# Performance work log

Measured on AMD Instinct MI355X. Metric: run time of the kernel, lower is better.

The kernel has to match this reference:

```python
import jax, jax.numpy as jnp
import numpy as np

K = 8192        # nodes (radio links)
DEG = 32        # out-degree per node
E = K * DEG
GE = 8          # graph_embedding_size
VAR = np.float32((10.0 ** (-19.9) * 5e6) / 10.0)  # output_noise_power / tx_power


def _init_mlp(key, dims_list):
    # per-node stacked Linear params, torch default init U(-1/sqrt(fan_in), 1/sqrt(fan_in))
    params = []
    for (din, dout) in dims_list:
        key, k1, k2 = jax.random.split(key, 3)
        b = float(1.0 / np.sqrt(din))
        params.append(jax.random.uniform(k1, (K, din, dout), minval=-b, maxval=b, dtype=jnp.float32))
        params.append(jax.random.uniform(k2, (K, dout), minval=-b, maxval=b, dtype=jnp.float32))
    return params


def setup_inputs() -> dict:
    key = jax.random.key(0)
    k = jax.random.split(key, 8)
    # edges sorted by src, exactly DEG distinct non-self out-neighbors per node
    src = jnp.repeat(jnp.arange(K), DEG)
    gaps = jax.random.randint(k[0], (K, DEG), 1, (K - 1) // DEG + 1)
    dst = ((jnp.arange(K)[:, None] + jnp.cumsum(gaps, axis=1)) % K).reshape(-1)
    edge_index = jnp.stack([src, dst])
    x = jax.random.uniform(k[1], (K, 1 + GE), dtype=jnp.float32)
    edge_attr = jax.random.uniform(k[2], (E, 1), dtype=jnp.float32)
    H = jax.random.uniform(k[3], (K, K), dtype=jnp.float32) * 1e-12  # |h_ij|^2 gains
    Wm1, bm1, Wm2, bm2 = _init_mlp(k[4], [(2 + GE, 32), (32, 32)])
    Wu1, bu1, Wu2, bu2 = _init_mlp(k[5], [(33 + GE, 16), (16, GE)])
    Wh1, bh1, Wh2, bh2 = _init_mlp(k[6], [(GE, 16), (16, 1)])
    return dict(x=x, edge_attr=edge_attr, H=H, edge_index=edge_index,
                Wm1=Wm1, bm1=bm1, Wm2=Wm2, bm2=bm2,
                Wu1=Wu1, bu1=bu1, Wu2=Wu2, bu2=bu2,
                Wh1=Wh1, bh1=bh1, Wh2=Wh2, bh2=bh2)


def reference(x, edge_attr, H, edge_index,
              Wm1, bm1, Wm2, bm2, Wu1, bu1, Wu2, bu2, Wh1, bh1, Wh2, bh2):
    src, dst = edge_index[0], edge_index[1]

    def conv(x):
        # message: tmp_e = [x[src_e], edge_attr_e]; node src's private mlp_m.
        # edges are contiguous groups of DEG per src -> grouped GEMM as batched einsum
        tmp = jnp.concatenate([x[src], edge_attr], axis=1).reshape(K, DEG, 2 + GE)
        h = jax.nn.relu(jnp.einsum('ked,kdh->keh', tmp, Wm1) + bm1[:, None])
        msg = jax.nn.relu(jnp.einsum('ked,kdh->keh', h, Wm2) + bm2[:, None])
        aggr = msg.sum(axis=1)                                  # [K,32] sum-aggregate
        t = jnp.concatenate([x, aggr], axis=1)                  # [K,41]
        u = jax.nn.relu(jnp.einsum('kd,kdh->kh', t, Wu1) + bu1)
        comb = jax.nn.relu(jnp.einsum('kd,kdh->kh', u, Wu2) + bu2)  # [K,8]
        return jnp.concatenate([x[:, :1], comb], axis=1)        # keep direct-channel col

    x3 = conv(conv(conv(x)))                                    # 3 rounds of LocalConv
    emb = x3[:, 1:]                                             # [K,8]
    hh = jax.nn.relu(jnp.einsum('kd,kdh->kh', emb, Wh1) + bh1)
    p = jax.nn.sigmoid(jnp.einsum('kd,kdh->kh', hh, Wh2) + bh2)[:, 0]  # power in (0,1)

    # per-node (negative) local rate over 1-hop out-neighborhood
    valid = p * jnp.diagonal(H)                                 # p_i * |h_ii|^2
    interf = jax.ops.segment_sum(p[dst] * H[src, dst], src, num_segments=K) + VAR
    interf = jax.lax.stop_gradient(interf)                      # .detach() in original
    local_rate = -jnp.log2(1.0 + valid / interf)                # [K]
    return local_rate
```

## Files before the change

kernel.cpp:

```cpp
#include <hip/hip_runtime.h>
#include <hip/hip_bf16.h>
#include <math.h>

#define KN 8192
#define DEG 32
#define EE (KN*DEG)

#define VAR_F 6.294627058970831e-15f

typedef __attribute__((ext_vector_type(8)))  short bf16x8;
typedef __attribute__((ext_vector_type(16))) float f32x16;

static __device__ __forceinline__ short bf_hi(float f) {
    __hip_bfloat16 h = __float2bfloat16(f);
    return __builtin_bit_cast(short, h);
}
static __device__ __forceinline__ float bf_f(short s) {
    __hip_bfloat16 h = __builtin_bit_cast(__hip_bfloat16, s);
    return __bfloat162float(h);
}

__global__ __launch_bounds__(64, 4) void mpnn_fused(
    const float* __restrict__ x,
    const float* __restrict__ edge_attr,
    const float* __restrict__ H,
    const int* __restrict__ edge_index,
    const float* __restrict__ Wm1, const float* __restrict__ bm1,
    const float* __restrict__ Wm2, const float* __restrict__ bm2,
    const float* __restrict__ Wu1, const float* __restrict__ bu1,
    const float* __restrict__ Wu2, const float* __restrict__ bu2,
    const float* __restrict__ Wh1, const float* __restrict__ bh1,
    const float* __restrict__ Wh2, const float* __restrict__ bh2,
    float* __restrict__ p_ws, float* __restrict__ valid_ws,
    float* __restrict__ hv_ws)
{
    __shared__ __align__(16) float c_lds[32];
    __shared__ float xt[44];
    __shared__ float ubuf[16];

    const int lane = threadIdx.x;
    const int col  = lane & 31;
    const int g    = lane >> 5;
    const int k    = blockIdx.x;

    const int m  = lane & 15;
    const int dg = lane >> 4;
    const int o  = lane & 7;
    const int mg = lane >> 3;

    const int* dstp = edge_index + EE;
    const int dv = dstp[k*DEG + col];
    const float Hv    = H[(size_t)k*KN + dv];
    const float Hdiag = H[(size_t)k*KN + k];

    const float a_e = edge_attr[k*32 + col];

    float wm1v[5];
    #pragma unroll
    for (int t = 0; t < 5; ++t) wm1v[t] = Wm1[(size_t)k*320 + t*64 + lane];

    float w9v[16];
    {
        const float* w9p = Wm1 + (size_t)k*320 + 288;
        float4 wa = *(const float4*)(w9p + g*8);
        float4 wb = *(const float4*)(w9p + g*8 + 4);
        float4 wc = *(const float4*)(w9p + 16 + g*8);
        float4 wd = *(const float4*)(w9p + 16 + g*8 + 4);
        w9v[0]=wa.x;  w9v[1]=wa.y;  w9v[2]=wa.z;  w9v[3]=wa.w;
        w9v[4]=wb.x;  w9v[5]=wb.y;  w9v[6]=wb.z;  w9v[7]=wb.w;
        w9v[8]=wc.x;  w9v[9]=wc.y;  w9v[10]=wc.z; w9v[11]=wc.w;
        w9v[12]=wd.x; w9v[13]=wd.y; w9v[14]=wd.z; w9v[15]=wd.w;
    }

    float wm2f[16];
    #pragma unroll
    for (int s = 0; s < 2; ++s)
        #pragma unroll
        for (int i = 0; i < 8; ++i)
            wm2f[s*8+i] = Wm2[(size_t)k*1024 + (s*16 + g*8 + i)*32 + col];

    const float bm1_i = bm1[k*32 + col];
    const float bm2_i = bm2[k*32 + col];

    float wu1v[10];
    #pragma unroll
    for (int t = 0; t < 10; ++t) wu1v[t] = Wu1[(size_t)k*656 + t*64 + lane];
    float wu1t = 0.f;
    if (lane < 16) wu1t = Wu1[(size_t)k*656 + 640 + lane];
    const float bu1_m = bu1[k*16 + m];

    const float wu2a  = Wu2[(size_t)k*128 + (mg*2+0)*8 + o];
    const float wu2b  = Wu2[(size_t)k*128 + (mg*2+1)*8 + o];
    const float bu2_o = bu2[k*8 + o];

    float wh1v[2];
    #pragma unroll
    for (int t = 0; t < 2; ++t) wh1v[t] = Wh1[(size_t)k*128 + t*64 + lane];
    const float bh1_m = bh1[k*16 + m];
    const float wh2_m = Wh2[k*16 + m];
    const float bh2_k = bh2[k];

    if (lane < 9) xt[lane] = x[(size_t)k*9 + lane];

    if (g == 0) hv_ws[k*DEG + col] = Hv;
    if (lane == 0) valid_ws[KN + k] = Hdiag;

    bf16x8 Bhi[2], Blo[2];
    #pragma unroll
    for (int s = 0; s < 2; ++s) {
        #pragma unroll
        for (int i = 0; i < 8; ++i) {
            float wv = wm2f[s*8+i];
            short h = bf_hi(wv);
            Bhi[s][i] = h;
            Blo[s][i] = bf_hi(wv - bf_f(h));
        }
    }

    for (int it = 0; it < 3; ++it) {
        float cpart = 0.f;
        #pragma unroll
        for (int t = 0; t < 4; ++t) cpart = fmaf(xt[2*t + g], wm1v[t], cpart);
        if (g == 0) cpart = fmaf(xt[8], wm1v[4], cpart);
        float c = bm1_i + cpart + __shfl_xor(cpart, 32);
        if (g == 0) c_lds[col] = c;

        const float4* cb = (const float4*)c_lds;
        float4 q0 = cb[g*2 + 0];
        float4 q1 = cb[g*2 + 1];
        float4 q2 = cb[4 + g*2 + 0];
        float4 q3 = cb[4 + g*2 + 1];
        float cv[16] = {q0.x,q0.y,q0.z,q0.w, q1.x,q1.y,q1.z,q1.w,
                        q2.x,q2.y,q2.z,q2.w, q3.x,q3.y,q3.z,q3.w};
        bf16x8 Ahi[2], Alo[2];
        #pragma unroll
        for (int s = 0; s < 2; ++s) {
            #pragma unroll
            for (int i = 0; i < 8; ++i) {
                int t = s*8 + i;
                float hv = fmaxf(fmaf(a_e, w9v[t], cv[t]), 0.f);
                short h = bf_hi(hv);
                Ahi[s][i] = h;
                Alo[s][i] = bf_hi(hv - bf_f(h));
            }
        }

        f32x16 acc;
        #pragma unroll
        for (int rr = 0; rr < 16; ++rr) acc[rr] = 0.f;
        #pragma unroll
        for (int s = 0; s < 2; ++s) {
            acc = __builtin_amdgcn_mfma_f32_32x32x16_bf16(Ahi[s], Bhi[s], acc, 0, 0, 0);
            acc = __builtin_amdgcn_mfma_f32_32x32x16_bf16(Ahi[s], Blo[s], acc, 0, 0, 0);
            acc = __builtin_amdgcn_mfma_f32_32x32x16_bf16(Alo[s], Bhi[s], acc, 0, 0, 0);
        }

        float ag = 0.f;
        #pragma unroll
        for (int rr = 0; rr < 16; ++rr) ag += fmaxf(acc[rr] + bm2_i, 0.f);
        ag += __shfl_xor(ag, 32);
        if (g == 0) xt[9 + col] = ag;

        float up = 0.f;
        #pragma unroll
        for (int t = 0; t < 10; ++t) up = fmaf(xt[4*t + dg], wu1v[t], up);
        up = fmaf(xt[40], wu1t, up);
        up += __shfl_xor(up, 16);
        up += __shfl_xor(up, 32);
        float u = fmaxf(up + bu1_m, 0.f);
        if (lane < 16) ubuf[lane] = u;

        float cp = wu2a * ubuf[mg*2] + wu2b * ubuf[mg*2 + 1];
        cp += __shfl_xor(cp, 8);
        cp += __shfl_xor(cp, 16);
        cp += __shfl_xor(cp, 32);
        float comb = fmaxf(cp + bu2_o, 0.f);
        if (lane < 8) xt[1 + lane] = comb;
    }

    float hp = fmaf(xt[1 + dg], wh1v[0], 0.f);
    hp = fmaf(xt[1 + 4 + dg], wh1v[1], hp);
    hp += __shfl_xor(hp, 16);
    hp += __shfl_xor(hp, 32);
    float hh = fmaxf(hp + bh1_m, 0.f);
    float pp = hh * wh2_m;
    pp += __shfl_xor(pp, 1);
    pp += __shfl_xor(pp, 2);
    pp += __shfl_xor(pp, 4);
    pp += __shfl_xor(pp, 8);
    float z = pp + bh2_k;
    float p = 1.f / (1.f + expf(-z));
    if (lane == 0) {
        p_ws[k] = p;
        valid_ws[k] = p * Hdiag;
    }
}

__global__ __launch_bounds__(256) void mpnn_interf(
    const int* __restrict__ edge_index,
    const float* __restrict__ p_ws,
    const float* __restrict__ valid_ws,
    const float* __restrict__ hv_ws,
    float* __restrict__ out)
{
    const int tid = threadIdx.x;
    const int s   = blockIdx.x * 32 + (tid >> 3);
    const int e4  = tid & 7;
    const int* dstp = edge_index + EE;

    int4   d4 = ((const int4*)  (dstp  + s*DEG))[e4];
    float4 h4 = ((const float4*)(hv_ws + s*DEG))[e4];
    float part = p_ws[d4.x] * h4.x + p_ws[d4.y] * h4.y
               + p_ws[d4.z] * h4.z + p_ws[d4.w] * h4.w;
    part += __shfl_xor(part, 1);
    part += __shfl_xor(part, 2);
    part += __shfl_xor(part, 4);
    if (e4 == 0) {
        float interf = part + VAR_F;
        out[s] = -log1pf(valid_ws[s] / interf) * 1.4426950408889634f;
    }
}

extern "C" void kernel_launch(void* const* d_in, const int* in_sizes, int n_in,
                              void* d_out, int out_size, void* d_ws, size_t ws_size,
                              hipStream_t stream) {
    const float* x         = (const float*)d_in[0];
    const float* edge_attr = (const float*)d_in[1];
    const float* H         = (const float*)d_in[2];
    const int*   edge_idx  = (const int*)  d_in[3];
    const float* Wm1 = (const float*)d_in[4];
    const float* bm1 = (const float*)d_in[5];
    const float* Wm2 = (const float*)d_in[6];
    const float* bm2 = (const float*)d_in[7];
    const float* Wu1 = (const float*)d_in[8];
    const float* bu1 = (const float*)d_in[9];
    const float* Wu2 = (const float*)d_in[10];
    const float* bu2 = (const float*)d_in[11];
    const float* Wh1 = (const float*)d_in[12];
    const float* bh1 = (const float*)d_in[13];
    const float* Wh2 = (const float*)d_in[14];
    const float* bh2 = (const float*)d_in[15];
    float* out = (float*)d_out;

    float* p_ws     = (float*)d_ws;
    float* valid_ws = p_ws + KN;
    float* hv_ws    = valid_ws + 2*KN;

    mpnn_fused<<<KN, 64, 0, stream>>>(x, edge_attr, H, edge_idx,
                                      Wm1, bm1, Wm2, bm2,
                                      Wu1, bu1, Wu2, bu2, Wh1, bh1, Wh2, bh2,
                                      p_ws, valid_ws, hv_ws);
    mpnn_interf<<<KN/32, 256, 0, stream>>>(edge_idx, p_ws, valid_ws,
                                           hv_ws, out);
}
```

Before: 29.93 us.

## Process four nodes per block with double-buffered LDS weight prefetch

Each workgroup now handles four consecutive nodes instead of one. It stages each node's per-node MLP weights and biases into a double-buffered LDS region with asynchronous global-to-LDS loads, so the next node's weights load while the current node computes. The launch shrinks to a quarter of the blocks and the launch-bounds occupancy hint drops from 4 to 2. The aim is to hide global memory latency on the weight streams, at the cost of fewer independent waves, serialized per-block work and more LDS per block.

New measurement: 36.76 us. 22.8% more time.

```diff
diff --git a/kernel.cpp b/kernel.cpp
--- a/kernel.cpp
+++ b/kernel.cpp
@@ -5,6 +5,8 @@
 #define KN 8192
 #define DEG 32
 #define EE (KN*DEG)
+#define NPW 4
+#define NBUF 2384
 
 #define VAR_F 6.294627058970831e-15f
 
@@ -20,7 +22,31 @@
     return __bfloat162float(h);
 }
 
-__global__ __launch_bounds__(64, 4) void mpnn_fused(
+static __device__ __forceinline__ void gl16(const float* src, float* lds) {
+    __builtin_amdgcn_global_load_lds(
+        (const __attribute__((address_space(1))) void*)src,
+        (__attribute__((address_space(3))) void*)lds, 16, 0, 0);
+}
+static __device__ __forceinline__ void gl4(const float* src, float* lds) {
+    __builtin_amdgcn_global_load_lds(
+        (const __attribute__((address_space(1))) void*)src,
+        (__attribute__((address_space(3))) void*)lds, 4, 0, 0);
+}
+
+#define O_WM1 0
+#define O_WM2 320
+#define O_WU1 1344
+#define O_WU2 2000
+#define O_WH1 2128
+#define O_BM1 2256
+#define O_BM2 2288
+#define O_BU1 2320
+#define O_BU2 2336
+#define O_BH1 2344
+#define O_WH2 2360
+#define O_BH2 2376
+
+__global__ __launch_bounds__(64, 2) void mpnn_fused(
     const float* __restrict__ x,
     const float* __restrict__ edge_attr,
     const float* __restrict__ H,
@@ -34,6 +60,7 @@
     float* __restrict__ p_ws, float* __restrict__ valid_ws,
     float* __restrict__ hv_ws)
 {
+    __shared__ __align__(16) float lbuf[2][NBUF];
     __shared__ __align__(16) float c_lds[32];
     __shared__ float xt[44];
     __shared__ float ubuf[16];
@@ -41,159 +68,198 @@
     const int lane = threadIdx.x;
     const int col  = lane & 31;
     const int g    = lane >> 5;
-    const int k    = blockIdx.x;
-
-    const int m  = lane & 15;
-    const int dg = lane >> 4;
-    const int o  = lane & 7;
-    const int mg = lane >> 3;
-
+    const int m    = lane & 15;
+    const int dg   = lane >> 4;
+    const int o    = lane & 7;
+    const int mg   = lane >> 3;
+    const int k0   = blockIdx.x * NPW;
     const int* dstp = edge_index + EE;
-    const int dv = dstp[k*DEG + col];
-    const float Hv    = H[(size_t)k*KN + dv];
-    const float Hdiag = H[(size_t)k*KN + k];
-
-    const float a_e = edge_attr[k*32 + col];
-
-    float wm1v[5];
-    #pragma unroll
-    for (int t = 0; t < 5; ++t) wm1v[t] = Wm1[(size_t)k*320 + t*64 + lane];
-
-    float w9v[16];
-    {
-        const float* w9p = Wm1 + (size_t)k*320 + 288;
-        float4 wa = *(const float4*)(w9p + g*8);
-        float4 wb = *(const float4*)(w9p + g*8 + 4);
-        float4 wc = *(const float4*)(w9p + 16 + g*8);
-        float4 wd = *(const float4*)(w9p + 16 + g*8 + 4);
-        w9v[0]=wa.x;  w9v[1]=wa.y;  w9v[2]=wa.z;  w9v[3]=wa.w;
-        w9v[4]=wb.x;  w9v[5]=wb.y;  w9v[6]=wb.z;  w9v[7]=wb.w;
-        w9v[8]=wc.x;  w9v[9]=wc.y;  w9v[10]=wc.z; w9v[11]=wc.w;
-        w9v[12]=wd.x; w9v[13]=wd.y; w9v[14]=wd.z; w9v[15]=wd.w;
-    }
-
-    float wm2f[16];
-    #pragma unroll
-    for (int s = 0; s < 2; ++s)
+
+    auto stage = [&](int k, float* B) {
+        const float* wm1p = Wm1 + (size_t)k*320;
+        gl16(wm1p + lane*4, B + O_WM1);
+        if (lane < 16) gl16(wm1p + 256 + lane*4, B + O_WM1 + 256);
+        const float* wm2p = Wm2 + (size_t)k*1024;
+        gl16(wm2p +       lane*4, B + O_WM2);
+        gl16(wm2p + 256 + lane*4, B + O_WM2 + 256);
+        gl16(wm2p + 512 + lane*4, B + O_WM2 + 512);
+        gl16(wm2p + 768 + lane*4, B + O_WM2 + 768);
+        const float* wu1p = Wu1 + (size_t)k*656;
+        gl16(wu1p +       lane*4, B + O_WU1);
+        gl16(wu1p + 256 + lane*4, B + O_WU1 + 256);
+        if (lane < 36) gl16(wu1p + 512 + lane*4, B + O_WU1 + 512);
+        if (lane < 32) gl16(Wu2 + (size_t)k*128 + lane*4, B + O_WU2);
+        if (lane < 32) gl16(Wh1 + (size_t)k*128 + lane*4, B + O_WH1);
+        if (lane < 8)  gl16(bm1 + (size_t)k*32  + lane*4, B + O_BM1);
+        if (lane < 8)  gl16(bm2 + (size_t)k*32  + lane*4, B + O_BM2);
+        if (lane < 4)  gl16(bu1 + (size_t)k*16  + lane*4, B + O_BU1);
+        if (lane < 2)  gl16(bu2 + (size_t)k*8   + lane*4, B + O_BU2);
+        if (lane < 4)  gl16(bh1 + (size_t)k*16  + lane*4, B + O_BH1);
+        if (lane < 4)  gl16(Wh2 + (size_t)k*16  + lane*4, B + O_WH2);
+        if (lane < 1)  gl4 (bh2 + k, B + O_BH2);
+    };
+
+    auto compute = [&](int k, const float* B, float a_e, float xval,
+                       float Hv, float Hd) {
+        if (lane < 9) xt[lane] = xval;
+
+        float wm1v[5];
         #pragma unroll
-        for (int i = 0; i < 8; ++i)
-            wm2f[s*8+i] = Wm2[(size_t)k*1024 + (s*16 + g*8 + i)*32 + col];
-
-    const float bm1_i = bm1[k*32 + col];
-    const float bm2_i = bm2[k*32 + col];
-
-    float wu1v[10];
-    #pragma unroll
-    for (int t = 0; t < 10; ++t) wu1v[t] = Wu1[(size_t)k*656 + t*64 + lane];
-    float wu1t = 0.f;
-    if (lane < 16) wu1t = Wu1[(size_t)k*656 + 640 + lane];
-    const float bu1_m = bu1[k*16 + m];
-
-    const float wu2a  = Wu2[(size_t)k*128 + (mg*2+0)*8 + o];
-    const float wu2b  = Wu2[(size_t)k*128 + (mg*2+1)*8 + o];
-    const float bu2_o = bu2[k*8 + o];
-
-    float wh1v[2];
-    #pragma unroll
-    for (int t = 0; t < 2; ++t) wh1v[t] = Wh1[(size_t)k*128 + t*64 + lane];
-    const float bh1_m = bh1[k*16 + m];
-    const float wh2_m = Wh2[k*16 + m];
-    const float bh2_k = bh2[k];
-
-    if (lane < 9) xt[lane] = x[(size_t)k*9 + lane];
-
-    if (g == 0) hv_ws[k*DEG + col] = Hv;
-    if (lane == 0) valid_ws[KN + k] = Hdiag;
-
-    bf16x8 Bhi[2], Blo[2];
-    #pragma unroll
-    for (int s = 0; s < 2; ++s) {
-        #pragma unroll
-        for (int i = 0; i < 8; ++i) {
-            float wv = wm2f[s*8+i];
-            short h = bf_hi(wv);
-            Bhi[s][i] = h;
-            Blo[s][i] = bf_hi(wv - bf_f(h));
+        for (int t = 0; t < 5; ++t) wm1v[t] = B[O_WM1 + t*64 + lane];
+
+        float w9v[16];
+        {
+            const float* w9p = B + O_WM1 + 288;
+            float4 wa = *(const float4*)(w9p + g*8);
+            float4 wb = *(const float4*)(w9p + g*8 + 4);
+            float4 wc = *(const float4*)(w9p + 16 + g*8);
+            float4 wd = *(const float4*)(w9p + 16 + g*8 + 4);
+            w9v[0]=wa.x;  w9v[1]=wa.y;  w9v[2]=wa.z;  w9v[3]=wa.w;
+            w9v[4]=wb.x;  w9v[5]=wb.y;  w9v[6]=wb.z;  w9v[7]=wb.w;
+            w9v[8]=wc.x;  w9v[9]=wc.y;  w9v[10]=wc.z; w9v[11]=wc.w;
+            w9v[12]=wd.x; w9v[13]=wd.y; w9v[14]=wd.z; w9v[15]=wd.w;
         }
-    }
-
-    for (int it = 0; it < 3; ++it) {
-        float cpart = 0.f;
-        #pragma unroll
-        for (int t = 0; t < 4; ++t) cpart = fmaf(xt[2*t + g], wm1v[t], cpart);
-        if (g == 0) cpart = fmaf(xt[8], wm1v[4], cpart);
-        float c = bm1_i + cpart + __shfl_xor(cpart, 32);
-        if (g == 0) c_lds[col] = c;
-
-        const float4* cb = (const float4*)c_lds;
-        float4 q0 = cb[g*2 + 0];
-        float4 q1 = cb[g*2 + 1];
-        float4 q2 = cb[4 + g*2 + 0];
-        float4 q3 = cb[4 + g*2 + 1];
-        float cv[16] = {q0.x,q0.y,q0.z,q0.w, q1.x,q1.y,q1.z,q1.w,
-                        q2.x,q2.y,q2.z,q2.w, q3.x,q3.y,q3.z,q3.w};
-        bf16x8 Ahi[2], Alo[2];
+
+        bf16x8 Bhi[2], Blo[2];
         #pragma unroll
         for (int s = 0; s < 2; ++s) {
             #pragma unroll
             for (int i = 0; i < 8; ++i) {
-                int t = s*8 + i;
-                float hv = fmaxf(fmaf(a_e, w9v[t], cv[t]), 0.f);
-                short h = bf_hi(hv);
-                Ahi[s][i] = h;
-                Alo[s][i] = bf_hi(hv - bf_f(h));
+                float wv = B[O_WM2 + (s*16 + g*8 + i)*32 + col];
+                short h = bf_hi(wv);
+                Bhi[s][i] = h;
+                Blo[s][i] = bf_hi(wv - bf_f(h));
             }
         }
 
-        f32x16 acc;
+        const float bm1_i = B[O_BM1 + col];
+        const float bm2_i = B[O_BM2 + col];
+
+        float wu1v[10];
         #pragma unroll
-        for (int rr = 0; rr < 16; ++rr) acc[rr] = 0.f;
+        for (int t = 0; t < 10; ++t) wu1v[t] = B[O_WU1 + t*64 + lane];
+        float wu1t = (lane < 16) ? B[O_WU1 + 640 + lane] : 0.f;
+        const float bu1_m = B[O_BU1 + m];
+
+        const float wu2a  = B[O_WU2 + (mg*2+0)*8 + o];
+        const float wu2b  = B[O_WU2 + (mg*2+1)*8 + o];
+        const float bu2_o = B[O_BU2 + o];
+
+        float wh1v[2];
         #pragma unroll
-        for (int s = 0; s < 2; ++s) {
-            acc = __builtin_amdgcn_mfma_f32_32x32x16_bf16(Ahi[s], Bhi[s], acc, 0, 0, 0);
-            acc = __builtin_amdgcn_mfma_f32_32x32x16_bf16(Ahi[s], Blo[s], acc, 0, 0, 0);
-            acc = __builtin_amdgcn_mfma_f32_32x32x16_bf16(Alo[s], Bhi[s], acc, 0, 0, 0);
+        for (int t = 0; t < 2; ++t) wh1v[t] = B[O_WH1 + t*64 + lane];
+        const float bh1_m = B[O_BH1 + m];
+        const float wh2_m = B[O_WH2 + m];
+        const float bh2_k = B[O_BH2];
+
+        for (int it = 0; it < 3; ++it) {
+            float cpart = 0.f;
+            #pragma unroll
+            for (int t = 0; t < 4; ++t) cpart = fmaf(xt[2*t + g], wm1v[t], cpart);
+            if (g == 0) cpart = fmaf(xt[8], wm1v[4], cpart);
+            float c = bm1_i + cpart + __shfl_xor(cpart, 32);
+            if (g == 0) c_lds[col] = c;
+
+            const float4* cb = (const float4*)c_lds;
+            float4 q0 = cb[g*2 + 0];
+            float4 q1 = cb[g*2 + 1];
+            float4 q2 = cb[4 + g*2 + 0];
+            float4 q3 = cb[4 + g*2 + 1];
+            float cv[16] = {q0.x,q0.y,q0.z,q0.w, q1.x,q1.y,q1.z,q1.w,
+                            q2.x,q2.y,q2.z,q2.w, q3.x,q3.y,q3.z,q3.w};
+            bf16x8 Ahi[2], Alo[2];
+            #pragma unroll
+            for (int s = 0; s < 2; ++s) {
+                #pragma unroll
+                for (int i = 0; i < 8; ++i) {
+                    int t = s*8 + i;
+                    float hv = fmaxf(fmaf(a_e, w9v[t], cv[t]), 0.f);
+                    short h = bf_hi(hv);
+                    Ahi[s][i] = h;
+                    Alo[s][i] = bf_hi(hv - bf_f(h));
+                }
+            }
+
+            f32x16 acc;
+            #pragma unroll
+            for (int rr = 0; rr < 16; ++rr) acc[rr] = 0.f;
+            #pragma unroll
+            for (int s = 0; s < 2; ++s) {
+                acc = __builtin_amdgcn_mfma_f32_32x32x16_bf16(Ahi[s], Bhi[s], acc, 0, 0, 0);
+                acc = __builtin_amdgcn_mfma_f32_32x32x16_bf16(Ahi[s], Blo[s], acc, 0, 0, 0);
+                acc = __builtin_amdgcn_mfma_f32_32x32x16_bf16(Alo[s], Bhi[s], acc, 0, 0, 0);
+            }
+
+            float ag = 0.f;
+            #pragma unroll
+            for (int rr = 0; rr < 16; ++rr) ag += fmaxf(acc[rr] + bm2_i, 0.f);
+            ag += __shfl_xor(ag, 32);
+            if (g == 0) xt[9 + col] = ag;
+
+            float up = 0.f;
+            #pragma unroll
+            for (int t = 0; t < 10; ++t) up = fmaf(xt[4*t + dg], wu1v[t], up);
+            up = fmaf(xt[40], wu1t, up);
+            up += __shfl_xor(up, 16);
+            up += __shfl_xor(up, 32);
+            float u = fmaxf(up + bu1_m, 0.f);
+            if (lane < 16) ubuf[lane] = u;
+
+            float cp = wu2a * ubuf[mg*2] + wu2b * ubuf[mg*2 + 1];
+            cp += __shfl_xor(cp, 8);
+            cp += __shfl_xor(cp, 16);
+            cp += __shfl_xor(cp, 32);
+            float comb = fmaxf(cp + bu2_o, 0.f);
+            if (lane < 8) xt[1 + lane] = comb;
         }
 
-        float ag = 0.f;
-        #pragma unroll
-        for (int rr = 0; rr < 16; ++rr) ag += fmaxf(acc[rr] + bm2_i, 0.f);
-        ag += __shfl_xor(ag, 32);
-        if (g == 0) xt[9 + col] = ag;
-
-        float up = 0.f;
-        #pragma unroll
-        for (int t = 0; t < 10; ++t) up = fmaf(xt[4*t + dg], wu1v[t], up);
-        up = fmaf(xt[40], wu1t, up);
-        up += __shfl_xor(up, 16);
-        up += __shfl_xor(up, 32);
-        float u = fmaxf(up + bu1_m, 0.f);
-        if (lane < 16) ubuf[lane] = u;
-
-        float cp = wu2a * ubuf[mg*2] + wu2b * ubuf[mg*2 + 1];
-        cp += __shfl_xor(cp, 8);
-        cp += __shfl_xor(cp, 16);
-        cp += __shfl_xor(cp, 32);
-        float comb = fmaxf(cp + bu2_o, 0.f);
-        if (lane < 8) xt[1 + lane] = comb;
+        float hp = fmaf(xt[1 + dg], wh1v[0], 0.f);
+        hp = fmaf(xt[1 + 4 + dg], wh1v[1], hp);
+        hp += __shfl_xor(hp, 16);
+        hp += __shfl_xor(hp, 32);
+        float hh = fmaxf(hp + bh1_m, 0.f);
+        float pp = hh * wh2_m;
+        pp += __shfl_xor(pp, 1);
+        pp += __shfl_xor(pp, 2);
+        pp += __shfl_xor(pp, 4);
+        pp += __shfl_xor(pp, 8);
+        float z = pp + bh2_k;
+        float p = 1.f / (1.f + expf(-z));
+
+        if (g == 0) hv_ws[k*DEG + col] = Hv;
+        if (lane == 0) {
+            p_ws[k] = p;
+            valid_ws[k] = p * Hd;
+        }
+    };
+
+    int dvv[NPW]; float Hdd[NPW], aev[NPW], xv[NPW];
+    #pragma unroll
+    for (int n = 0; n < NPW; ++n) {
+        int kk = k0 + n;
+        dvv[n] = dstp[kk*DEG + col];
+        Hdd[n] = H[(size_t)kk*KN + kk];
+        aev[n] = edge_attr[kk*32 + col];
+        xv[n]  = (lane < 9) ? x[(size_t)kk*9 + lane] : 0.f;
     }
 
-    float hp = fmaf(xt[1 + dg], wh1v[0], 0.f);
-    hp = fmaf(xt[1 + 4 + dg], wh1v[1], hp);
-    hp += __shfl_xor(hp, 16);
-    hp += __shfl_xor(hp, 32);
-    float hh = fmaxf(hp + bh1_m, 0.f);
-    float pp = hh * wh2_m;
-    pp += __shfl_xor(pp, 1);
-    pp += __shfl_xor(pp, 2);
-    pp += __shfl_xor(pp, 4);
-    pp += __shfl_xor(pp, 8);
-    float z = pp + bh2_k;
-    float p = 1.f / (1.f + expf(-z));
-    if (lane == 0) {
-        p_ws[k] = p;
-        valid_ws[k] = p * Hdiag;
-    }
+    stage(k0 + 0, lbuf[0]);
+
+    float Hvv[NPW];
+    #pragma unroll
+    for (int n = 0; n < NPW; ++n)
+        Hvv[n] = H[(size_t)(k0 + n)*KN + dvv[n]];
+
+    stage(k0 + 1, lbuf[1]);
+
+    compute(k0 + 0, lbuf[0], aev[0], xv[0], Hvv[0], Hdd[0]);
+    __builtin_amdgcn_sched_barrier(0);
+    stage(k0 + 2, lbuf[0]);
+    compute(k0 + 1, lbuf[1], aev[1], xv[1], Hvv[1], Hdd[1]);
+    __builtin_amdgcn_sched_barrier(0);
+    stage(k0 + 3, lbuf[1]);
+    compute(k0 + 2, lbuf[0], aev[2], xv[2], Hvv[2], Hdd[2]);
+    compute(k0 + 3, lbuf[1], aev[3], xv[3], Hvv[3], Hdd[3]);
 }
 
 __global__ __launch_bounds__(256) void mpnn_interf(
@@ -246,10 +312,10 @@
     float* valid_ws = p_ws + KN;
     float* hv_ws    = valid_ws + 2*KN;
 
-    mpnn_fused<<<KN, 64, 0, stream>>>(x, edge_attr, H, edge_idx,
-                                      Wm1, bm1, Wm2, bm2,
-                                      Wu1, bu1, Wu2, bu2, Wh1, bh1, Wh2, bh2,
-                                      p_ws, valid_ws, hv_ws);
+    mpnn_fused<<<KN/NPW, 64, 0, stream>>>(x, edge_attr, H, edge_idx,
+                                          Wm1, bm1, Wm2, bm2,
+                                          Wu1, bu1, Wu2, bu2, Wh1, bh1, Wh2, bh2,
+                                          p_ws, valid_ws, hv_ws);
     mpnn_interf<<<KN/32, 256, 0, stream>>>(edge_idx, p_ws, valid_ws,
                                            hv_ws, out);
 }
```

## Process two nodes per block with async global-to-LDS Wm2 prefetch

Applied to the files above, without the earlier changes.

Each 64-thread block now handles two nodes in sequence instead of one, halving the grid. Both nodes' Wm2 matrices are loaded up front with global_load_lds into two LDS buffers, and their Wm1/Wu1 weights are loaded together, so the second node's weights arrive while the first node computes. The unused Hdiag copy in the workspace is removed. The cost is fewer blocks to hide latency, 8KB of LDS per block, more registers, and no explicit wait or barrier before the LDS weights are read, which relies on the compiler inserting the vmcnt wait.

Measured after the change: 35.87 us. +19.9%, slower.

```diff
diff --git a/kernel.cpp b/kernel.cpp
--- a/kernel.cpp
+++ b/kernel.cpp
@@ -18,6 +18,12 @@
 static __device__ __forceinline__ float bf_f(short s) {
     __hip_bfloat16 h = __builtin_bit_cast(__hip_bfloat16, s);
     return __bfloat162float(h);
+}
+
+static __device__ __forceinline__ void gl16(const float* src, float* lds) {
+    __builtin_amdgcn_global_load_lds(
+        (const __attribute__((address_space(1))) void*)src,
+        (__attribute__((address_space(3))) void*)lds, 16, 0, 0);
 }
 
 __global__ __launch_bounds__(64, 4) void mpnn_fused(
@@ -34,6 +40,8 @@
     float* __restrict__ p_ws, float* __restrict__ valid_ws,
     float* __restrict__ hv_ws)
 {
+    __shared__ __align__(16) float LB0[1024];
+    __shared__ __align__(16) float LB1[1024];
     __shared__ __align__(16) float c_lds[32];
     __shared__ float xt[44];
     __shared__ float ubuf[16];
@@ -41,159 +49,175 @@
     const int lane = threadIdx.x;
     const int col  = lane & 31;
     const int g    = lane >> 5;
-    const int k    = blockIdx.x;
-
-    const int m  = lane & 15;
-    const int dg = lane >> 4;
-    const int o  = lane & 7;
-    const int mg = lane >> 3;
-
+    const int m    = lane & 15;
+    const int dg   = lane >> 4;
+    const int o    = lane & 7;
+    const int mg   = lane >> 3;
+    const int k0   = blockIdx.x * 2;
     const int* dstp = edge_index + EE;
-    const int dv = dstp[k*DEG + col];
-    const float Hv    = H[(size_t)k*KN + dv];
-    const float Hdiag = H[(size_t)k*KN + k];
-
-    const float a_e = edge_attr[k*32 + col];
-
-    float wm1v[5];
+
+    const int   dv0 = dstp[k0*DEG + col];
+    const int   dv1 = dstp[(k0+1)*DEG + col];
+    const float Hd0 = H[(size_t)k0*KN + k0];
+    const float Hd1 = H[(size_t)(k0+1)*KN + (k0+1)];
+    const float ae0 = edge_attr[k0*32 + col];
+    const float ae1 = edge_attr[(k0+1)*32 + col];
+    const float xv0 = (lane < 9) ? x[(size_t)k0*9 + lane] : 0.f;
+    const float xv1 = (lane < 9) ? x[(size_t)(k0+1)*9 + lane] : 0.f;
+
+    {
+        const float* wp = Wm2 + (size_t)k0*1024;
+        gl16(wp +       lane*4, LB0);
+        gl16(wp + 256 + lane*4, LB0 + 256);
+        gl16(wp + 512 + lane*4, LB0 + 512);
+        gl16(wp + 768 + lane*4, LB0 + 768);
+        const float* wq = wp + 1024;
+        gl16(wq +       lane*4, LB1);
+        gl16(wq + 256 + lane*4, LB1 + 256);
+        gl16(wq + 512 + lane*4, LB1 + 512);
+        gl16(wq + 768 + lane*4, LB1 + 768);
+    }
+
+    float wm1vA[5], wm1vB[5];
     #pragma unroll
-    for (int t = 0; t < 5; ++t) wm1v[t] = Wm1[(size_t)k*320 + t*64 + lane];
-
-    float w9v[16];
-    {
-        const float* w9p = Wm1 + (size_t)k*320 + 288;
-        float4 wa = *(const float4*)(w9p + g*8);
-        float4 wb = *(const float4*)(w9p + g*8 + 4);
-        float4 wc = *(const float4*)(w9p + 16 + g*8);
-        float4 wd = *(const float4*)(w9p + 16 + g*8 + 4);
-        w9v[0]=wa.x;  w9v[1]=wa.y;  w9v[2]=wa.z;  w9v[3]=wa.w;
-        w9v[4]=wb.x;  w9v[5]=wb.y;  w9v[6]=wb.z;  w9v[7]=wb.w;
-        w9v[8]=wc.x;  w9v[9]=wc.y;  w9v[10]=wc.z; w9v[11]=wc.w;
-        w9v[12]=wd.x; w9v[13]=wd.y; w9v[14]=wd.z; w9v[15]=wd.w;
-    }
-
-    float wm2f[16];
+    for (int t = 0; t < 5; ++t) {
+        wm1vA[t] = Wm1[(size_t)k0*320 + t*64 + lane];
+        wm1vB[t] = Wm1[(size_t)(k0+1)*320 + t*64 + lane];
+    }
+    float wu1vA[10], wu1vB[10];
     #pragma unroll
-    for (int s = 0; s < 2; ++s)
-        #pragma unroll
-        for (int i = 0; i < 8; ++i)
-            wm2f[s*8+i] = Wm2[(size_t)k*1024 + (s*16 + g*8 + i)*32 + col];
-
-    const float bm1_i = bm1[k*32 + col];
-    const float bm2_i = bm2[k*32 + col];
-
-    float wu1v[10];
-    #pragma unroll
-    for (int t = 0; t < 10; ++t) wu1v[t] = Wu1[(size_t)k*656 + t*64 + lane];
-    float wu1t = 0.f;
-    if (lane < 16) wu1t = Wu1[(size_t)k*656 + 640 + lane];
-    const float bu1_m = bu1[k*16 + m];
-
-    const float wu2a  = Wu2[(size_t)k*128 + (mg*2+0)*8 + o];
-    const float wu2b  = Wu2[(size_t)k*128 + (mg*2+1)*8 + o];
-    const float bu2_o = bu2[k*8 + o];
-
-    float wh1v[2];
-    #pragma unroll
-    for (int t = 0; t < 2; ++t) wh1v[t] = Wh1[(size_t)k*128 + t*64 + lane];
-    const float bh1_m = bh1[k*16 + m];
-    const float wh2_m = Wh2[k*16 + m];
-    const float bh2_k = bh2[k];
-
-    if (lane < 9) xt[lane] = x[(size_t)k*9 + lane];
-
-    if (g == 0) hv_ws[k*DEG + col] = Hv;
-    if (lane == 0) valid_ws[KN + k] = Hdiag;
-
-    bf16x8 Bhi[2], Blo[2];
-    #pragma unroll
-    for (int s = 0; s < 2; ++s) {
-        #pragma unroll
-        for (int i = 0; i < 8; ++i) {
-            float wv = wm2f[s*8+i];
-            short h = bf_hi(wv);
-            Bhi[s][i] = h;
-            Blo[s][i] = bf_hi(wv - bf_f(h));
-        }
-    }
-
-    for (int it = 0; it < 3; ++it) {
-        float cpart = 0.f;
-        #pragma unroll
-        for (int t = 0; t < 4; ++t) cpart = fmaf(xt[2*t + g], wm1v[t], cpart);
-        if (g == 0) cpart = fmaf(xt[8], wm1v[4], cpart);
-        float c = bm1_i + cpart + __shfl_xor(cpart, 32);
-        if (g == 0) c_lds[col] = c;
-
-        const float4* cb = (const float4*)c_lds;
-        float4 q0 = cb[g*2 + 0];
-        float4 q1 = cb[g*2 + 1];
-        float4 q2 = cb[4 + g*2 + 0];
-        float4 q3 = cb[4 + g*2 + 1];
-        float cv[16] = {q0.x,q0.y,q0.z,q0.w, q1.x,q1.y,q1.z,q1.w,
-                        q2.x,q2.y,q2.z,q2.w, q3.x,q3.y,q3.z,q3.w};
-        bf16x8 Ahi[2], Alo[2];
+    for (int t = 0; t < 10; ++t) {
+        wu1vA[t] = Wu1[(size_t)k0*656 + t*64 + lane];
+        wu1vB[t] = Wu1[(size_t)(k0+1)*656 + t*64 + lane];
+    }
+
+    auto compute = [&](int k, const float* WB, const float* wm1v,
+                       const float* wu1v, float a_e, float xval,
+                       int dvv, float Hd) {
+        const float Hv = H[(size_t)k*KN + dvv];
+
+        float w9v[16];
+        {
+            const float* w9p = Wm1 + (size_t)k*320 + 288;
+            float4 wa = *(const float4*)(w9p + g*8);
+            float4 wb = *(const float4*)(w9p + g*8 + 4);
+            float4 wc = *(const float4*)(w9p + 16 + g*8);
+            float4 wd = *(const float4*)(w9p + 16 + g*8 + 4);
+            w9v[0]=wa.x;  w9v[1]=wa.y;  w9v[2]=wa.z;  w9v[3]=wa.w;
+            w9v[4]=wb.x;  w9v[5]=wb.y;  w9v[6]=wb.z;  w9v[7]=wb.w;
+            w9v[8]=wc.x;  w9v[9]=wc.y;  w9v[10]=wc.z; w9v[11]=wc.w;
+            w9v[12]=wd.x; w9v[13]=wd.y; w9v[14]=wd.z; w9v[15]=wd.w;
+        }
+        const float bm1_i = bm1[k*32 + col];
+        const float bm2_i = bm2[k*32 + col];
+        const float wu1t  = (lane < 16) ? Wu1[(size_t)k*656 + 640 + lane] : 0.f;
+        const float bu1_m = bu1[k*16 + m];
+        const float wu2a  = Wu2[(size_t)k*128 + (mg*2+0)*8 + o];
+        const float wu2b  = Wu2[(size_t)k*128 + (mg*2+1)*8 + o];
+        const float bu2_o = bu2[k*8 + o];
+        const float wh1v0 = Wh1[(size_t)k*128 + lane];
+        const float wh1v1 = Wh1[(size_t)k*128 + 64 + lane];
+        const float bh1_m = bh1[k*16 + m];
+        const float wh2_m = Wh2[k*16 + m];
+        const float bh2_k = bh2[k];
+
+        if (lane < 9) xt[lane] = xval;
+
+        bf16x8 Bhi[2], Blo[2];
         #pragma unroll
         for (int s = 0; s < 2; ++s) {
             #pragma unroll
             for (int i = 0; i < 8; ++i) {
-                int t = s*8 + i;
-                float hv = fmaxf(fmaf(a_e, w9v[t], cv[t]), 0.f);
-                short h = bf_hi(hv);
-                Ahi[s][i] = h;
-                Alo[s][i] = bf_hi(hv - bf_f(h));
+                float wv = WB[(s*16 + g*8 + i)*32 + col];
+                short h = bf_hi(wv);
+                Bhi[s][i] = h;
+                Blo[s][i] = bf_hi(wv - bf_f(h));
             }
         }
 
-        f32x16 acc;
-        #pragma unroll
-        for (int rr = 0; rr < 16; ++rr) acc[rr] = 0.f;
-        #pragma unroll
-        for (int s = 0; s < 2; ++s) {
-            acc = __builtin_amdgcn_mfma_f32_32x32x16_bf16(Ahi[s], Bhi[s], acc, 0, 0, 0);
-            acc = __builtin_amdgcn_mfma_f32_32x32x16_bf16(Ahi[s], Blo[s], acc, 0, 0, 0);
-            acc = __builtin_amdgcn_mfma_f32_32x32x16_bf16(Alo[s], Bhi[s], acc, 0, 0, 0);
-        }
-
-        float ag = 0.f;
-        #pragma unroll
-        for (int rr = 0; rr < 16; ++rr) ag += fmaxf(acc[rr] + bm2_i, 0.f);
-        ag += __shfl_xor(ag, 32);
-        if (g == 0) xt[9 + col] = ag;
-
-        float up = 0.f;
-        #pragma unroll
-        for (int t = 0; t < 10; ++t) up = fmaf(xt[4*t + dg], wu1v[t], up);
-        up = fmaf(xt[40], wu1t, up);
-        up += __shfl_xor(up, 16);
-        up += __shfl_xor(up, 32);
-        float u = fmaxf(up + bu1_m, 0.f);
-        if (lane < 16) ubuf[lane] = u;
-
-        float cp = wu2a * ubuf[mg*2] + wu2b * ubuf[mg*2 + 1];
-        cp += __shfl_xor(cp, 8);
-        cp += __shfl_xor(cp, 16);
-        cp += __shfl_xor(cp, 32);
-        float comb = fmaxf(cp + bu2_o, 0.f);
-        if (lane < 8) xt[1 + lane] = comb;
-    }
-
-    float hp = fmaf(xt[1 + dg], wh1v[0], 0.f);
-    hp = fmaf(xt[1 + 4 + dg], wh1v[1], hp);
-    hp += __shfl_xor(hp, 16);
-    hp += __shfl_xor(hp, 32);
-    float hh = fmaxf(hp + bh1_m, 0.f);
-    float pp = hh * wh2_m;
-    pp += __shfl_xor(pp, 1);
-    pp += __shfl_xor(pp, 2);
-    pp += __shfl_xor(pp, 4);
-    pp += __shfl_xor(pp, 8);
-    float z = pp + bh2_k;
-    float p = 1.f / (1.f + expf(-z));
-    if (lane == 0) {
-        p_ws[k] = p;
-        valid_ws[k] = p * Hdiag;
-    }
+        for (int it = 0; it < 3; ++it) {
+            float cpart = 0.f;
+            #pragma unroll
+            for (int t = 0; t < 4; ++t) cpart = fmaf(xt[2*t + g], wm1v[t], cpart);
+            if (g == 0) cpart = fmaf(xt[8], wm1v[4], cpart);
+            float c = bm1_i + cpart + __shfl_xor(cpart, 32);
+            if (g == 0) c_lds[col] = c;
+
+            const float4* cb = (const float4*)c_lds;
+            float4 q0 = cb[g*2 + 0];
+            float4 q1 = cb[g*2 + 1];
+            float4 q2 = cb[4 + g*2 + 0];
+            float4 q3 = cb[4 + g*2 + 1];
+            float cv[16] = {q0.x,q0.y,q0.z,q0.w, q1.x,q1.y,q1.z,q1.w,
+                            q2.x,q2.y,q2.z,q2.w, q3.x,q3.y,q3.z,q3.w};
+            bf16x8 Ahi[2], Alo[2];
+            #pragma unroll
+            for (int s = 0; s < 2; ++s) {
+                #pragma unroll
+                for (int i = 0; i < 8; ++i) {
+                    int t = s*8 + i;
+                    float hv = fmaxf(fmaf(a_e, w9v[t], cv[t]), 0.f);
+                    short h = bf_hi(hv);
+                    Ahi[s][i] = h;
+                    Alo[s][i] = bf_hi(hv - bf_f(h));
+                }
+            }
+
+            f32x16 acc;
+            #pragma unroll
+            for (int rr = 0; rr < 16; ++rr) acc[rr] = 0.f;
+            #pragma unroll
+            for (int s = 0; s < 2; ++s) {
+                acc = __builtin_amdgcn_mfma_f32_32x32x16_bf16(Ahi[s], Bhi[s], acc, 0, 0, 0);
+                acc = __builtin_amdgcn_mfma_f32_32x32x16_bf16(Ahi[s], Blo[s], acc, 0, 0, 0);
+                acc = __builtin_amdgcn_mfma_f32_32x32x16_bf16(Alo[s], Bhi[s], acc, 0, 0, 0);
+            }
+
+            float ag = 0.f;
+            #pragma unroll
+            for (int rr = 0; rr < 16; ++rr) ag += fmaxf(acc[rr] + bm2_i, 0.f);
+            ag += __shfl_xor(ag, 32);
+            if (g == 0) xt[9 + col] = ag;
+
+            float up = 0.f;
+            #pragma unroll
+            for (int t = 0; t < 10; ++t) up = fmaf(xt[4*t + dg], wu1v[t], up);
+            up = fmaf(xt[40], wu1t, up);
+            up += __shfl_xor(up, 16);
+            up += __shfl_xor(up, 32);
+            float u = fmaxf(up + bu1_m, 0.f);
+            if (lane < 16) ubuf[lane] = u;
+
+            float cp = wu2a * ubuf[mg*2] + wu2b * ubuf[mg*2 + 1];
+            cp += __shfl_xor(cp, 8);
+            cp += __shfl_xor(cp, 16);
+            cp += __shfl_xor(cp, 32);
+            float comb = fmaxf(cp + bu2_o, 0.f);
+            if (lane < 8) xt[1 + lane] = comb;
+        }
+
+        float hp = fmaf(xt[1 + dg], wh1v0, 0.f);
+        hp = fmaf(xt[1 + 4 + dg], wh1v1, hp);
+        hp += __shfl_xor(hp, 16);
+        hp += __shfl_xor(hp, 32);
+        float hh = fmaxf(hp + bh1_m, 0.f);
+        float pp = hh * wh2_m;
+        pp += __shfl_xor(pp, 1);
+        pp += __shfl_xor(pp, 2);
+        pp += __shfl_xor(pp, 4);
+        pp += __shfl_xor(pp, 8);
+        float z = pp + bh2_k;
+        float p = 1.f / (1.f + expf(-z));
+
+        if (g == 0) hv_ws[k*DEG + col] = Hv;
+        if (lane == 0) {
+            p_ws[k] = p;
+            valid_ws[k] = p * Hd;
+        }
+    };
+
+    compute(k0,     LB0, wm1vA, wu1vA, ae0, xv0, dv0, Hd0);
+    compute(k0 + 1, LB1, wm1vB, wu1vB, ae1, xv1, dv1, Hd1);
 }
 
 __global__ __launch_bounds__(256) void mpnn_interf(
@@ -244,12 +268,12 @@
 
     float* p_ws     = (float*)d_ws;
     float* valid_ws = p_ws + KN;
-    float* hv_ws    = valid_ws + 2*KN;
-
-    mpnn_fused<<<KN, 64, 0, stream>>>(x, edge_attr, H, edge_idx,
-                                      Wm1, bm1, Wm2, bm2,
-                                      Wu1, bu1, Wu2, bu2, Wh1, bh1, Wh2, bh2,
-                                      p_ws, valid_ws, hv_ws);
+    float* hv_ws    = valid_ws + KN;
+
+    mpnn_fused<<<KN/2, 64, 0, stream>>>(x, edge_attr, H, edge_idx,
+                                        Wm1, bm1, Wm2, bm2,
+                                        Wu1, bu1, Wu2, bu2, Wh1, bh1, Wh2, bh2,
+                                        p_ws, valid_ws, hv_ws);
     mpnn_interf<<<KN/32, 256, 0, stream>>>(edge_idx, p_ws, valid_ws,
                                            hv_ws, out);
 }
```
